# Kernel tuning notes

Measured on AMD Instinct MI355X. Metric: run time of the kernel, lower is better.

Reference implementation:

```python
import jax, jax.numpy as jnp
import numpy as np

IMG_W = 224
STRIDE = 16
NUM_HEADS = 12
# 196 grid centers, x-major order: [(x, y) for x in ... for y in ...]
_xs = np.arange(STRIDE // 2, IMG_W, STRIDE)
GRIDS = jnp.asarray(np.array([(x, y) for x in _xs for y in _xs], dtype=np.float32))  # [196, 2]


def setup_inputs() -> dict:
    key = jax.random.key(0)
    ks = jax.random.split(key, 8)
    B, N, C = 256, 198, 768
    s = 0.02
    return {
        "x": jax.random.normal(ks[0], (B, N, C), dtype=jnp.float32),
        "w_qkv": jax.random.normal(ks[1], (C, 3 * C), dtype=jnp.float32) * s,  # qkv_bias=False
        "w_proj": jax.random.normal(ks[2], (C, C), dtype=jnp.float32) * s,
        "b_proj": jax.random.normal(ks[3], (C,), dtype=jnp.float32) * s,
        "w_D": jax.random.normal(ks[4], (C, 3), dtype=jnp.float32) * s,
        "b_D": jax.random.normal(ks[5], (3,), dtype=jnp.float32) * s,
        "w_cen": jax.random.normal(ks[6], (C, 6), dtype=jnp.float32) * s,
        "b_cen": jax.random.normal(ks[7], (6,), dtype=jnp.float32) * s,
    }


def reference(x, w_qkv, w_proj, b_proj, w_D, b_D, w_cen, b_cen):
    B, N, C = x.shape
    H = NUM_HEADS
    dh = C // H
    scale = dh ** (-0.5)

    qkv = (x @ w_qkv).reshape(B, N, 3, H, dh).transpose(2, 0, 3, 1, 4)  # [3,B,H,N,dh]
    q, k, v = qkv[0], qkv[1], qkv[2]

    attn = jnp.einsum('bhnd,bhmd->bhnm', q, k) * scale
    attn = jax.nn.softmax(attn, axis=-1)  # [B,H,N,N]

    # CLS-token query, heads concatenated: q.permute(2,0,1,3).reshape(N,B,C)[0]
    q0 = q[:, :, 0, :].reshape(B, C)
    D = IMG_W * jax.nn.sigmoid(q0 @ w_D + b_D)                      # [B,3]
    cen = jax.nn.sigmoid((q0 @ w_cen + b_cen).reshape(B, 3, 2))     # [B,3,2]

    # mixture-of-gaussian blobs over 196 patch grid positions
    sigma = (D / 2.0)[..., None]                                    # [B,3,1]
    coord = cen * (IMG_W - 1)                                       # [B,3,2]
    dist = ((coord[:, :, None, :] - GRIDS[None, None]) ** 2).sum(-1)  # [B,3,196]
    mgb = jnp.exp(-dist / (2.0 * sigma ** 2)) / 2.0 / 3.14 / sigma ** 2
    mgb = mgb / mgb.sum(-1, keepdims=True)
    mgb = mgb.sum(axis=1) / 3.0                                     # [B,196]
    mgb = jnp.concatenate([jnp.ones((B, 2), mgb.dtype), mgb], axis=1)  # [B,N]

    # head-score reweighting of the CLS attention row
    hs = attn[:, :, 0, :].transpose(1, 0, 2)   # [H,B,N] == permute(1,2,0,3) squeezed
    hs = hs * mgb[None]                        # broadcast over heads
    hs = hs / hs.sum(-1, keepdims=True)
    # replicate torch masked_scatter flat-order semantics:
    # source flattened in (h,b,n) order is written into target positions in (b,h,n) order
    new_row = hs.reshape(-1).reshape(B, H, N)
    attn = attn.at[:, :, 0, :].set(new_row)

    out = jnp.einsum('bhnm,bhmd->bhnd', attn, v)      # [B,H,N,dh]
    out = out.transpose(0, 2, 1, 3).reshape(B, N, C)
    out = out @ w_proj + b_proj
    return cen, attn[:, :, 0, :], out
```

## Files before the change

kernel.cpp:

```cpp
#include <hip/hip_runtime.h>
#include <cstdint>
#include <cstddef>

typedef __attribute__((ext_vector_type(4))) float  f32x4;
typedef __attribute__((ext_vector_type(8))) __bf16 bf16x8;
typedef __attribute__((ext_vector_type(4))) __bf16 bf16x4;

#define MFMA16(A, B, C) __builtin_amdgcn_mfma_f32_16x16x32_bf16((A), (B), (C), 0, 0, 0)

#define GLOAD_LDS16(gp, lp)                                        \
    __builtin_amdgcn_global_load_lds(                              \
        (const __attribute__((address_space(1))) void*)(gp),       \
        (__attribute__((address_space(3))) void*)(lp), 16, 0, 0)

#define NB 256
#define NN 198
#define NC 768
#define NH 12

__global__ __launch_bounds__(256) void cast_to_bf16(const float* __restrict__ in,
                                                    __bf16* __restrict__ out, int n8) {
    int i = blockIdx.x * 256 + threadIdx.x;
    if (i < n8) {
        const float4 f0 = reinterpret_cast<const float4*>(in)[i * 2];
        const float4 f1 = reinterpret_cast<const float4*>(in)[i * 2 + 1];
        bf16x8 h;
        h[0] = (__bf16)f0.x; h[1] = (__bf16)f0.y; h[2] = (__bf16)f0.z; h[3] = (__bf16)f0.w;
        h[4] = (__bf16)f1.x; h[5] = (__bf16)f1.y; h[6] = (__bf16)f1.z; h[7] = (__bf16)f1.w;
        reinterpret_cast<bf16x8*>(out)[i] = h;
    }
}

__global__ __launch_bounds__(256) void transpose_to_bf16(
    const float* __restrict__ in, __bf16* __restrict__ out, int R, int Cc) {
    __shared__ __bf16 tile[32][33];
    const int ntc = Cc >> 5;
    const int tc = blockIdx.x % ntc, tr = blockIdx.x / ntc;
    const int c0 = tc * 32, r0 = tr * 32;
    const int lx = threadIdx.x & 31, ly = threadIdx.x >> 5;
#pragma unroll
    for (int j = 0; j < 4; ++j)
        tile[ly + j * 8][lx] = (__bf16)in[(size_t)(r0 + ly + j * 8) * Cc + c0 + lx];
    __syncthreads();
#pragma unroll
    for (int j = 0; j < 4; ++j)
        out[(size_t)(c0 + ly + j * 8) * R + r0 + lx] = tile[lx][ly + j * 8];
}

__global__ __launch_bounds__(512, 2) void gemm_qkv_v7(
    const __bf16* __restrict__ xb, const __bf16* __restrict__ wT,
    __bf16* __restrict__ qb, __bf16* __restrict__ kb, __bf16* __restrict__ vb,
    float* __restrict__ q0) {
    __shared__ __bf16 As[2][256 * 64];
    __shared__ __bf16 Bs[2][256 * 64];
    const int bid = blockIdx.x;
    const int xcd = bid & 7, lin = bid >> 3;
    const int wgid = (xcd < 6 ? xcd * 223 : 6 * 223 + (xcd - 6) * 222) + lin;
    const int brow = (wgid / 9) * 256;
    const int bcol = (wgid % 9) * 256;
    const int tid = threadIdx.x, lane = tid & 63, wid = tid >> 6;
    const int wr = wid >> 2, wc = wid & 3;
    const int lr = lane & 15, lg = lane >> 4;

    const int srow = tid >> 3;
    const int sslot = (tid & 7) ^ ((tid >> 3) & 7);
    const __bf16* aSrc = xb + (size_t)(brow + srow) * 768 + sslot * 8;
    const __bf16* bSrc = wT + (size_t)(bcol + srow) * 768 + sslot * 8;
    const int key = lr & 7;

    f32x4 acc[8][4] = {};

#define STAGE7(buf, kk0)                                                       \
    {                                                                          \
        __bf16* aD = &As[buf][wid * 512];                                      \
        __bf16* bD = &Bs[buf][wid * 512];                                      \
        _Pragma("unroll")                                                      \
        for (int j = 0; j < 4; ++j) {                                          \
            GLOAD_LDS16(aSrc + (size_t)j * 64 * 768 + (kk0), aD + j * 4096);   \
            GLOAD_LDS16(bSrc + (size_t)j * 64 * 768 + (kk0), bD + j * 4096);   \
        }                                                                      \
    }

#define LDA7(f0, f1, f2, f3, m0)                                               \
    f0 = *reinterpret_cast<const bf16x8*>(                                     \
        Ab + (wr * 128 + (m0) * 16 + lr) * 64 + ((lg ^ key) * 8));             \
    f1 = *reinterpret_cast<const bf16x8*>(                                     \
        Ab + (wr * 128 + (m0) * 16 + lr) * 64 + (((4 + lg) ^ key) * 8));       \
    f2 = *reinterpret_cast<const bf16x8*>(                                     \
        Ab + (wr * 128 + (m0) * 16 + 16 + lr) * 64 + ((lg ^ key) * 8));        \
    f3 = *reinterpret_cast<const bf16x8*>(                                     \
        Ab + (wr * 128 + (m0) * 16 + 16 + lr) * 64 + (((4 + lg) ^ key) * 8));

#define MFMA_PHASE7(f0, f1, f2, f3, m0)                                        \
    __builtin_amdgcn_s_setprio(1);                                             \
    _Pragma("unroll")                                                          \
    for (int nt = 0; nt < 4; ++nt) acc[(m0)][nt]     = MFMA16(f0, bfr[0][nt], acc[(m0)][nt]);     \
    _Pragma("unroll")                                                          \
    for (int nt = 0; nt < 4; ++nt) acc[(m0)][nt]     = MFMA16(f1, bfr[1][nt], acc[(m0)][nt]);     \
    _Pragma("unroll")                                                          \
    for (int nt = 0; nt < 4; ++nt) acc[(m0) + 1][nt] = MFMA16(f2, bfr[0][nt], acc[(m0) + 1][nt]); \
    _Pragma("unroll")                                                          \
    for (int nt = 0; nt < 4; ++nt) acc[(m0) + 1][nt] = MFMA16(f3, bfr[1][nt], acc[(m0) + 1][nt]); \
    __builtin_amdgcn_s_setprio(0);

    STAGE7(0, 0);
    STAGE7(1, 64);
    for (int tau = 0; tau < 12; ++tau) {
        const int b = tau & 1;
        if (tau == 11) asm volatile("s_waitcnt vmcnt(0)" ::: "memory");
        else           asm volatile("s_waitcnt vmcnt(8)" ::: "memory");
        __builtin_amdgcn_s_barrier();
        __builtin_amdgcn_sched_barrier(0);
        const __bf16* Ab = As[b];
        const __bf16* Bb = Bs[b];
        bf16x8 bfr[2][4];
#pragma unroll
        for (int kk = 0; kk < 2; ++kk)
#pragma unroll
            for (int nt = 0; nt < 4; ++nt)
                bfr[kk][nt] = *reinterpret_cast<const bf16x8*>(
                    Bb + (wc * 64 + nt * 16 + lr) * 64 + (((kk * 4 + lg) ^ key) * 8));
        bf16x8 a0, a1, a2, a3, b0, b1, b2, b3;
        LDA7(a0, a1, a2, a3, 0);
        LDA7(b0, b1, b2, b3, 2);
        asm volatile("s_waitcnt lgkmcnt(4)" ::: "memory");
        __builtin_amdgcn_sched_barrier(0);
        MFMA_PHASE7(a0, a1, a2, a3, 0);
        LDA7(a0, a1, a2, a3, 4);
        asm volatile("s_waitcnt lgkmcnt(4)" ::: "memory");
        __builtin_amdgcn_sched_barrier(0);
        MFMA_PHASE7(b0, b1, b2, b3, 2);
        LDA7(b0, b1, b2, b3, 6);
        asm volatile("s_waitcnt lgkmcnt(4)" ::: "memory");
        __builtin_amdgcn_sched_barrier(0);
        MFMA_PHASE7(a0, a1, a2, a3, 4);
        asm volatile("s_waitcnt lgkmcnt(0)" ::: "memory");
        __builtin_amdgcn_sched_barrier(0);
        __builtin_amdgcn_s_barrier();
        __builtin_amdgcn_sched_barrier(0);
        if (tau < 10) STAGE7(b, (tau + 2) * 64);
        MFMA_PHASE7(b0, b1, b2, b3, 6);
    }
#undef STAGE7

#pragma unroll
    for (int mt = 0; mt < 8; ++mt) {
        int grow0 = brow + wr * 128 + mt * 16 + lg * 4;
#pragma unroll
        for (int nt = 0; nt < 4; ++nt) {
            int gcol = bcol + wc * 64 + nt * 16 + lr;
            int sidx = gcol / 768;
            int rem  = gcol % 768;
            __bf16* dstbuf = (sidx == 0) ? qb : (sidx == 1) ? kb : vb;
            int hh = rem >> 6, dd = rem & 63;
#pragma unroll
            for (int r = 0; r < 4; ++r) {
                int grow = grow0 + r;
                int bb = grow / 198, nn2 = grow % 198;
                float val = acc[mt][nt][r];
                dstbuf[(((size_t)bb * 12 + hh) * 198 + nn2) * 64 + dd] = (__bf16)val;
                if (sidx == 0 && nn2 == 0) q0[bb * 768 + rem] = val;
            }
        }
    }
}

__global__ __launch_bounds__(256) void mgb_kernel(
    const float* __restrict__ q0, const float* __restrict__ wD,
    const float* __restrict__ bD, const float* __restrict__ wcen,
    const float* __restrict__ bcen, float* __restrict__ cen_out,
    float* __restrict__ mgb) {
    const int b = blockIdx.x, t = threadIdx.x;
    __shared__ float qs[768];
    __shared__ float red[256];
    __shared__ float vals[9];
    qs[t]       = q0[b * 768 + t];
    qs[t + 256] = q0[b * 768 + t + 256];
    qs[t + 512] = q0[b * 768 + t + 512];
    __syncthreads();
    for (int j = 0; j < 9; ++j) {
        float p;
        if (j < 3)
            p = qs[t] * wD[t * 3 + j] + qs[t + 256] * wD[(t + 256) * 3 + j] +
                qs[t + 512] * wD[(t + 512) * 3 + j];
        else {
            int c = j - 3;
            p = qs[t] * wcen[t * 6 + c] + qs[t + 256] * wcen[(t + 256) * 6 + c] +
                qs[t + 512] * wcen[(t + 512) * 6 + c];
        }
        red[t] = p;
        __syncthreads();
        for (int off = 128; off > 0; off >>= 1) {
            if (t < off) red[t] += red[t + off];
            __syncthreads();
        }
        if (t == 0) {
            float bias = (j < 3) ? bD[j] : bcen[j - 3];
            vals[j] = 1.f / (1.f + __expf(-(red[0] + bias)));
        }
        __syncthreads();
    }
    if (t < 6) cen_out[b * 6 + t] = vals[3 + t];

    float e3[3] = {0.f, 0.f, 0.f};
    if (t < 196) {
        float gx = 8.f + 16.f * (float)(t / 14);
        float gy = 8.f + 16.f * (float)(t % 14);
#pragma unroll
        for (int j = 0; j < 3; ++j) {
            float sig = 112.f * vals[j];
            float cx = vals[3 + 2 * j] * 223.f;
            float cy = vals[3 + 2 * j + 1] * 223.f;
            float dx = cx - gx, dy = cy - gy;
            e3[j] = __expf(-(dx * dx + dy * dy) / (2.f * sig * sig));
        }
    }
    float js[3];
    for (int j = 0; j < 3; ++j) {
        red[t] = e3[j];
        __syncthreads();
        for (int off = 128; off > 0; off >>= 1) {
            if (t < off) red[t] += red[t + off];
            __syncthreads();
        }
        js[j] = red[0];
        __syncthreads();
    }
    if (t < 196) {
        float m = (e3[0] / js[0] + e3[1] / js[1] + e3[2] / js[2]) * (1.f / 3.f);
        mgb[(size_t)b * 198 + 2 + t] = m;
    }
    if (t < 2) mgb[(size_t)b * 198 + t] = 1.f;
}

__global__ __launch_bounds__(256) void attn_kernel(
    const __bf16* __restrict__ qb, const __bf16* __restrict__ kb,
    const __bf16* __restrict__ vb, float* __restrict__ p0,
    __bf16* __restrict__ outp) {
    __shared__ __bf16 Vt[64][216];
    __shared__ __bf16 Plds[4][16][216];
    const int bh = blockIdx.x;
    const int b = bh / 12, h = bh % 12;
    const __bf16* Qp = qb + (size_t)bh * NN * 64;
    const __bf16* Kp = kb + (size_t)bh * NN * 64;
    const __bf16* Vp = vb + (size_t)bh * NN * 64;
    const int tid = threadIdx.x, lane = tid & 63, wid = tid >> 6;
    const int lr = lane & 15, lg = lane >> 4;

    for (int i = tid; i < 104 * 8; i += 256) {
        int key2 = (i >> 3) * 2, d0 = (i & 7) << 3;
        int kr0 = key2 < 198 ? key2 : 197;
        int kr1 = key2 + 1 < 198 ? key2 + 1 : 197;
        bf16x8 h0 = *reinterpret_cast<const bf16x8*>(Vp + kr0 * 64 + d0);
        bf16x8 h1 = *reinterpret_cast<const bf16x8*>(Vp + kr1 * 64 + d0);
#pragma unroll
        for (int j = 0; j < 8; ++j) {
            union { __bf16 hh[2]; unsigned u; } pk;
            pk.hh[0] = h0[j]; pk.hh[1] = h1[j];
            *reinterpret_cast<unsigned*>(&Vt[d0 + j][key2]) = pk.u;
        }
    }
    __syncthreads();

    for (int ch = wid; ch < 13; ch += 4) {
        int n0 = ch * 16;
        int qrow = n0 + lr; if (qrow > 197) qrow = 197;
        bf16x8 qf0 = *reinterpret_cast<const bf16x8*>(Qp + qrow * 64 + lg * 8);
        bf16x8 qf1 = *reinterpret_cast<const bf16x8*>(Qp + qrow * 64 + 32 + lg * 8);
        f32x4 sa[13];
#pragma unroll
        for (int t2 = 0; t2 < 13; ++t2) {
            int krow = t2 * 16 + lr; if (krow > 197) krow = 197;
            bf16x8 kf0 = *reinterpret_cast<const bf16x8*>(Kp + krow * 64 + lg * 8);
            bf16x8 kf1 = *reinterpret_cast<const bf16x8*>(Kp + krow * 64 + 32 + lg * 8);
            f32x4 a = (f32x4){0.f, 0.f, 0.f, 0.f};
            a = MFMA16(kf0, qf0, a);
            a = MFMA16(kf1, qf1, a);
            sa[t2] = a;
        }
        float rmax = -1e30f;
#pragma unroll
        for (int t2 = 0; t2 < 13; ++t2)
#pragma unroll
            for (int r = 0; r < 4; ++r) {
                int key = t2 * 16 + lg * 4 + r;
                float vv = (key < 198) ? sa[t2][r] * 0.125f : -1e30f;
                sa[t2][r] = vv;
                rmax = fmaxf(rmax, vv);
            }
        rmax = fmaxf(rmax, __shfl_xor(rmax, 16));
        rmax = fmaxf(rmax, __shfl_xor(rmax, 32));
        float rsum = 0.f;
#pragma unroll
        for (int t2 = 0; t2 < 13; ++t2)
#pragma unroll
            for (int r = 0; r < 4; ++r) {
                float e = __expf(sa[t2][r] - rmax);
                sa[t2][r] = e;
                rsum += e;
            }
        rsum += __shfl_xor(rsum, 16);
        rsum += __shfl_xor(rsum, 32);
        float inv = 1.f / rsum;

        if (ch == 0 && lr == 0) {
#pragma unroll
            for (int t2 = 0; t2 < 13; ++t2)
#pragma unroll
                for (int r = 0; r < 4; ++r) {
                    int key = t2 * 16 + lg * 4 + r;
                    if (key < 198) p0[(size_t)bh * 198 + key] = sa[t2][r] * inv;
                }
        }
#pragma unroll
        for (int t2 = 0; t2 < 13; ++t2) {
            bf16x4 pk;
#pragma unroll
            for (int r = 0; r < 4; ++r) pk[r] = (__bf16)(sa[t2][r] * inv);
            *reinterpret_cast<bf16x4*>(&Plds[wid][lr][t2 * 16 + lg * 4]) = pk;
        }
        asm volatile("s_waitcnt lgkmcnt(0)" ::: "memory");

        f32x4 o[4];
#pragma unroll
        for (int mt = 0; mt < 4; ++mt) o[mt] = (f32x4){0.f, 0.f, 0.f, 0.f};
#pragma unroll
        for (int ks = 0; ks < 7; ++ks) {
            int kbase = ks * 32 + lg * 8;
            bf16x8 pf;
            if (kbase < 208)
                pf = *reinterpret_cast<const bf16x8*>(&Plds[wid][lr][kbase]);
            else {
#pragma unroll
                for (int j = 0; j < 8; ++j) pf[j] = (__bf16)0.f;
            }
#pragma unroll
            for (int mt = 0; mt < 4; ++mt) {
                bf16x8 vf;
                if (kbase < 208)
                    vf = *reinterpret_cast<const bf16x8*>(&Vt[mt * 16 + lr][kbase]);
                else {
#pragma unroll
                    for (int j = 0; j < 8; ++j) vf[j] = (__bf16)0.f;
                }
                o[mt] = MFMA16(vf, pf, o[mt]);
            }
        }
        int qg = n0 + lr;
        if (qg < 198) {
            __bf16* dst = outp + ((size_t)b * 198 + qg) * 768 + h * 64;
#pragma unroll
            for (int mt = 0; mt < 4; ++mt) {
                bf16x4 pk;
#pragma unroll
                for (int r = 0; r < 4; ++r) pk[r] = (__bf16)o[mt][r];
                *reinterpret_cast<bf16x4*>(dst + mt * 16 + lg * 4) = pk;
            }
        }
    }
}

__global__ __launch_bounds__(64) void reweight_kernel(
    const float* __restrict__ p0, const float* __restrict__ mgb,
    const __bf16* __restrict__ vb, float* __restrict__ attn_out,
    __bf16* __restrict__ outp) {
    const int t = blockIdx.x;
    const int b = t / 12, h = t % 12;
    const int h2 = t >> 8, b2 = t & 255;
    const int lane = threadIdx.x;
    __shared__ float nr[198];
    const float* pr = p0 + (size_t)(b2 * 12 + h2) * 198;
    const float* mr = mgb + (size_t)b2 * 198;
    float w[4];
    float ssum = 0.f;
#pragma unroll
    for (int i = 0; i < 4; ++i) {
        int n = lane + 64 * i;
        float xv = (n < 198) ? pr[n] * mr[n] : 0.f;
        w[i] = xv;
        ssum += xv;
    }
#pragma unroll
    for (int m = 1; m < 64; m <<= 1) ssum += __shfl_xor(ssum, m);
    float inv = 1.f / ssum;
#pragma unroll
    for (int i = 0; i < 4; ++i) {
        int n = lane + 64 * i;
        if (n < 198) {
            float xv = w[i] * inv;
            nr[n] = xv;
            attn_out[(size_t)t * 198 + n] = xv;
        }
    }
    __syncthreads();
    const __bf16* vp = vb + (size_t)t * 198 * 64;
    float acc = 0.f;
    for (int n = 0; n < 198; ++n) acc += nr[n] * (float)vp[n * 64 + lane];
    outp[((size_t)b * 198) * 768 + h * 64 + lane] = (__bf16)acc;
}

__global__ __launch_bounds__(512, 2) void gemm_proj_v7(
    const __bf16* __restrict__ A, const __bf16* __restrict__ wT,
    const float* __restrict__ bias, float* __restrict__ out) {
    __shared__ __bf16 As[2][256 * 64];
    __shared__ __bf16 Bs[2][256 * 64];
    const int bid = blockIdx.x;
    const int xcd = bid & 7, lin = bid >> 3;
    const int wgid = (xcd < 2 ? xcd * 75 : 2 * 75 + (xcd - 2) * 74) + lin;
    const int brow = (wgid / 3) * 256;
    const int bcol = (wgid % 3) * 256;
    const int tid = threadIdx.x, lane = tid & 63, wid = tid >> 6;
    const int wr = wid >> 2, wc = wid & 3;
    const int lr = lane & 15, lg = lane >> 4;

    const int srow = tid >> 3;
    const int sslot = (tid & 7) ^ ((tid >> 3) & 7);
    const __bf16* aSrc = A  + (size_t)(brow + srow) * 768 + sslot * 8;
    const __bf16* bSrc = wT + (size_t)(bcol + srow) * 768 + sslot * 8;
    const int key = lr & 7;

    f32x4 acc[8][4] = {};

#define STAGE8(buf, kk0)                                                       \
    {                                                                          \
        __bf16* aD = &As[buf][wid * 512];                                      \
        __bf16* bD = &Bs[buf][wid * 512];                                      \
        _Pragma("unroll")                                                      \
        for (int j = 0; j < 4; ++j) {                                          \
            GLOAD_LDS16(aSrc + (size_t)j * 64 * 768 + (kk0), aD + j * 4096);   \
            GLOAD_LDS16(bSrc + (size_t)j * 64 * 768 + (kk0), bD + j * 4096);   \
        }                                                                      \
    }

    STAGE8(0, 0);
    STAGE8(1, 64);
    for (int tau = 0; tau < 12; ++tau) {
        const int b = tau & 1;
        if (tau == 11) asm volatile("s_waitcnt vmcnt(0)" ::: "memory");
        else           asm volatile("s_waitcnt vmcnt(8)" ::: "memory");
        __builtin_amdgcn_s_barrier();
        __builtin_amdgcn_sched_barrier(0);
        const __bf16* Ab = As[b];
        const __bf16* Bb = Bs[b];
        bf16x8 bfr[2][4];
#pragma unroll
        for (int kk = 0; kk < 2; ++kk)
#pragma unroll
            for (int nt = 0; nt < 4; ++nt)
                bfr[kk][nt] = *reinterpret_cast<const bf16x8*>(
                    Bb + (wc * 64 + nt * 16 + lr) * 64 + (((kk * 4 + lg) ^ key) * 8));
        bf16x8 a0, a1, a2, a3, b0, b1, b2, b3;
        LDA7(a0, a1, a2, a3, 0);
        LDA7(b0, b1, b2, b3, 2);
        asm volatile("s_waitcnt lgkmcnt(4)" ::: "memory");
        __builtin_amdgcn_sched_barrier(0);
        MFMA_PHASE7(a0, a1, a2, a3, 0);
        LDA7(a0, a1, a2, a3, 4);
        asm volatile("s_waitcnt lgkmcnt(4)" ::: "memory");
        __builtin_amdgcn_sched_barrier(0);
        MFMA_PHASE7(b0, b1, b2, b3, 2);
        LDA7(b0, b1, b2, b3, 6);
        asm volatile("s_waitcnt lgkmcnt(4)" ::: "memory");
        __builtin_amdgcn_sched_barrier(0);
        MFMA_PHASE7(a0, a1, a2, a3, 4);
        asm volatile("s_waitcnt lgkmcnt(0)" ::: "memory");
        __builtin_amdgcn_sched_barrier(0);
        __builtin_amdgcn_s_barrier();
        __builtin_amdgcn_sched_barrier(0);
        if (tau < 10) STAGE8(b, (tau + 2) * 64);
        MFMA_PHASE7(b0, b1, b2, b3, 6);
    }
#undef STAGE8

#pragma unroll
    for (int mt = 0; mt < 8; ++mt) {
#pragma unroll
        for (int nt = 0; nt < 4; ++nt) {
            int gcol = bcol + wc * 64 + nt * 16 + lr;
            float bv = bias[gcol];
#pragma unroll
            for (int r = 0; r < 4; ++r) {
                int grow = brow + wr * 128 + mt * 16 + lg * 4 + r;
                out[(size_t)grow * 768 + gcol] = acc[mt][nt][r] + bv;
            }
        }
    }
}

extern "C" void kernel_launch(void* const* d_in, const int* in_sizes, int n_in,
                              void* d_out, int out_size, void* d_ws, size_t ws_size,
                              hipStream_t stream) {
    const float* x      = (const float*)d_in[0];
    const float* w_qkv  = (const float*)d_in[1];
    const float* w_proj = (const float*)d_in[2];
    const float* b_proj = (const float*)d_in[3];
    const float* w_D    = (const float*)d_in[4];
    const float* b_D    = (const float*)d_in[5];
    const float* w_cen  = (const float*)d_in[6];
    const float* b_cen  = (const float*)d_in[7];

    float* out      = (float*)d_out;
    float* cen_out  = out;
    float* attn_out = out + 1536;
    float* proj_out = out + 1536 + 608256;

    char* ws = (char*)d_ws;
    size_t off = 0;
    auto carve = [&](size_t bytes) {
        void* p = ws + off;
        off += (bytes + 255) & ~(size_t)255;
        return p;
    };
    __bf16* wqkvT  = (__bf16*)carve((size_t)2304 * 768 * 2);
    __bf16* wprojT = (__bf16*)carve((size_t)768 * 768 * 2);
    __bf16* qb     = (__bf16*)carve((size_t)3072 * 198 * 64 * 2);
    __bf16* kb     = (__bf16*)carve((size_t)3072 * 198 * 64 * 2);
    __bf16* vb     = (__bf16*)carve((size_t)3072 * 198 * 64 * 2);
    __bf16* outp   = (__bf16*)carve((size_t)50688 * 768 * 2);
    float*  q0     = (float*)carve((size_t)256 * 768 * 4);
    float*  mgb    = (float*)carve((size_t)256 * 198 * 4);
    float*  p0     = (float*)carve((size_t)3072 * 198 * 4);

    __bf16* xb = outp;

    cast_to_bf16<<<(50688 * 768 / 8 + 255) / 256, 256, 0, stream>>>(x, xb, 50688 * 768 / 8);
    transpose_to_bf16<<<(2304 / 32) * (768 / 32), 256, 0, stream>>>(w_qkv, wqkvT, 768, 2304);
    transpose_to_bf16<<<(768 / 32) * (768 / 32), 256, 0, stream>>>(w_proj, wprojT, 768, 768);
    gemm_qkv_v7<<<1782, 512, 0, stream>>>(xb, wqkvT, qb, kb, vb, q0);
    mgb_kernel<<<256, 256, 0, stream>>>(q0, w_D, b_D, w_cen, b_cen, cen_out, mgb);
    attn_kernel<<<3072, 256, 0, stream>>>(qb, kb, vb, p0, outp);
    reweight_kernel<<<3072, 64, 0, stream>>>(p0, mgb, vb, attn_out, outp);
    gemm_proj_v7<<<594, 512, 0, stream>>>(outp, wprojT, b_proj, proj_out);
}
```

Before: 524.0 us.

## Pair query chunks for shared K fragments in attention; retile projection GEMM to 128x128

In the attention kernel each wave now computes QK^T for two query chunks at once, so every K fragment loaded from global memory feeds both chunks and K traffic is roughly halved. Softmax and PV move into a shared helper. Separately, the projection GEMM is rebuilt with 128x128 tiles, a K step of 32, 256 threads and 2376 blocks, plus s_setprio around the MFMAs. This trades per-block data reuse for more blocks and higher occupancy, while the attention change raises register pressure.

```diff
diff --git a/kernel.cpp b/kernel.cpp
--- a/kernel.cpp
+++ b/kernel.cpp
@@ -233,6 +233,91 @@
     if (t < 2) mgb[(size_t)b * 198 + t] = 1.f;
 }
 
+__device__ __forceinline__ void softmax_pv(
+    f32x4 (&sa)[13], int ch, int wid, int lr, int lg, int bh, int b, int h,
+    float* __restrict__ p0, __bf16* __restrict__ outp,
+    __bf16 (&Vt)[64][216], __bf16 (&Plds)[4][16][216]) {
+    float rmax = -1e30f;
+#pragma unroll
+    for (int t2 = 0; t2 < 13; ++t2)
+#pragma unroll
+        for (int r = 0; r < 4; ++r) {
+            int key = t2 * 16 + lg * 4 + r;
+            float vv = (key < 198) ? sa[t2][r] * 0.125f : -1e30f;
+            sa[t2][r] = vv;
+            rmax = fmaxf(rmax, vv);
+        }
+    rmax = fmaxf(rmax, __shfl_xor(rmax, 16));
+    rmax = fmaxf(rmax, __shfl_xor(rmax, 32));
+    float rsum = 0.f;
+#pragma unroll
+    for (int t2 = 0; t2 < 13; ++t2)
+#pragma unroll
+        for (int r = 0; r < 4; ++r) {
+            float e = __expf(sa[t2][r] - rmax);
+            sa[t2][r] = e;
+            rsum += e;
+        }
+    rsum += __shfl_xor(rsum, 16);
+    rsum += __shfl_xor(rsum, 32);
+    float inv = 1.f / rsum;
+
+    if (ch == 0 && lr == 0) {
+#pragma unroll
+        for (int t2 = 0; t2 < 13; ++t2)
+#pragma unroll
+            for (int r = 0; r < 4; ++r) {
+                int key = t2 * 16 + lg * 4 + r;
+                if (key < 198) p0[(size_t)bh * 198 + key] = sa[t2][r] * inv;
+            }
+    }
+#pragma unroll
+    for (int t2 = 0; t2 < 13; ++t2) {
+        bf16x4 pk;
+#pragma unroll
+        for (int r = 0; r < 4; ++r) pk[r] = (__bf16)(sa[t2][r] * inv);
+        *reinterpret_cast<bf16x4*>(&Plds[wid][lr][t2 * 16 + lg * 4]) = pk;
+    }
+    asm volatile("s_waitcnt lgkmcnt(0)" ::: "memory");
+
+    f32x4 o[4];
+#pragma unroll
+    for (int mt = 0; mt < 4; ++mt) o[mt] = (f32x4){0.f, 0.f, 0.f, 0.f};
+#pragma unroll
+    for (int ks = 0; ks < 7; ++ks) {
+        int kbase = ks * 32 + lg * 8;
+        bf16x8 pf;
+        if (kbase < 208)
+            pf = *reinterpret_cast<const bf16x8*>(&Plds[wid][lr][kbase]);
+        else {
+#pragma unroll
+            for (int j = 0; j < 8; ++j) pf[j] = (__bf16)0.f;
+        }
+#pragma unroll
+        for (int mt = 0; mt < 4; ++mt) {
+            bf16x8 vf;
+            if (kbase < 208)
+                vf = *reinterpret_cast<const bf16x8*>(&Vt[mt * 16 + lr][kbase]);
+            else {
+#pragma unroll
+                for (int j = 0; j < 8; ++j) vf[j] = (__bf16)0.f;
+            }
+            o[mt] = MFMA16(vf, pf, o[mt]);
+        }
+    }
+    int qg = ch * 16 + lr;
+    if (qg < 198) {
+        __bf16* dst = outp + ((size_t)b * 198 + qg) * 768 + h * 64;
+#pragma unroll
+        for (int mt = 0; mt < 4; ++mt) {
+            bf16x4 pk;
+#pragma unroll
+            for (int r = 0; r < 4; ++r) pk[r] = (__bf16)o[mt][r];
+            *reinterpret_cast<bf16x4*>(dst + mt * 16 + lg * 4) = pk;
+        }
+    }
+}
+
 __global__ __launch_bounds__(256) void attn_kernel(
     const __bf16* __restrict__ qb, const __bf16* __restrict__ kb,
     const __bf16* __restrict__ vb, float* __restrict__ p0,
@@ -262,101 +347,37 @@
     }
     __syncthreads();
 
-    for (int ch = wid; ch < 13; ch += 4) {
-        int n0 = ch * 16;
-        int qrow = n0 + lr; if (qrow > 197) qrow = 197;
-        bf16x8 qf0 = *reinterpret_cast<const bf16x8*>(Qp + qrow * 64 + lg * 8);
-        bf16x8 qf1 = *reinterpret_cast<const bf16x8*>(Qp + qrow * 64 + 32 + lg * 8);
-        f32x4 sa[13];
+#pragma unroll
+    for (int pp = 0; pp < 2; ++pp) {
+        const int c0 = wid + pp * 8;
+        const int c1 = c0 + 4;
+        const bool has1 = (c1 < 13);
+        int qrow0 = c0 * 16 + lr; if (qrow0 > 197) qrow0 = 197;
+        bf16x8 qf00 = *reinterpret_cast<const bf16x8*>(Qp + qrow0 * 64 + lg * 8);
+        bf16x8 qf01 = *reinterpret_cast<const bf16x8*>(Qp + qrow0 * 64 + 32 + lg * 8);
+        int qrow1 = has1 ? c1 * 16 + lr : 197; if (qrow1 > 197) qrow1 = 197;
+        bf16x8 qf10 = *reinterpret_cast<const bf16x8*>(Qp + qrow1 * 64 + lg * 8);
+        bf16x8 qf11 = *reinterpret_cast<const bf16x8*>(Qp + qrow1 * 64 + 32 + lg * 8);
+        f32x4 sa0[13], sa1[13];
 #pragma unroll
         for (int t2 = 0; t2 < 13; ++t2) {
             int krow = t2 * 16 + lr; if (krow > 197) krow = 197;
             bf16x8 kf0 = *reinterpret_cast<const bf16x8*>(Kp + krow * 64 + lg * 8);
             bf16x8 kf1 = *reinterpret_cast<const bf16x8*>(Kp + krow * 64 + 32 + lg * 8);
             f32x4 a = (f32x4){0.f, 0.f, 0.f, 0.f};
-            a = MFMA16(kf0, qf0, a);
-            a = MFMA16(kf1, qf1, a);
-            sa[t2] = a;
-        }
-        float rmax = -1e30f;
-#pragma unroll
-        for (int t2 = 0; t2 < 13; ++t2)
-#pragma unroll
-            for (int r = 0; r < 4; ++r) {
-                int key = t2 * 16 + lg * 4 + r;
-                float vv = (key < 198) ? sa[t2][r] * 0.125f : -1e30f;
-                sa[t2][r] = vv;
-                rmax = fmaxf(rmax, vv);
+            a = MFMA16(kf0, qf00, a);
+            a = MFMA16(kf1, qf01, a);
+            sa0[t2] = a;
+            if (has1) {
+                f32x4 c = (f32x4){0.f, 0.f, 0.f, 0.f};
+                c = MFMA16(kf0, qf10, c);
+                c = MFMA16(kf1, qf11, c);
+                sa1[t2] = c;
             }
-        rmax = fmaxf(rmax, __shfl_xor(rmax, 16));
-        rmax = fmaxf(rmax, __shfl_xor(rmax, 32));
-        float rsum = 0.f;
-#pragma unroll
-        for (int t2 = 0; t2 < 13; ++t2)
-#pragma unroll
-            for (int r = 0; r < 4; ++r) {
-                float e = __expf(sa[t2][r] - rmax);
-                sa[t2][r] = e;
-                rsum += e;
-            }
-        rsum += __shfl_xor(rsum, 16);
-        rsum += __shfl_xor(rsum, 32);
-        float inv = 1.f / rsum;
-
-        if (ch == 0 && lr == 0) {
-#pragma unroll
-            for (int t2 = 0; t2 < 13; ++t2)
-#pragma unroll
-                for (int r = 0; r < 4; ++r) {
-                    int key = t2 * 16 + lg * 4 + r;
-                    if (key < 198) p0[(size_t)bh * 198 + key] = sa[t2][r] * inv;
-                }
-        }
-#pragma unroll
-        for (int t2 = 0; t2 < 13; ++t2) {
-            bf16x4 pk;
-#pragma unroll
-            for (int r = 0; r < 4; ++r) pk[r] = (__bf16)(sa[t2][r] * inv);
-            *reinterpret_cast<bf16x4*>(&Plds[wid][lr][t2 * 16 + lg * 4]) = pk;
-        }
-        asm volatile("s_waitcnt lgkmcnt(0)" ::: "memory");
-
-        f32x4 o[4];
-#pragma unroll
-        for (int mt = 0; mt < 4; ++mt) o[mt] = (f32x4){0.f, 0.f, 0.f, 0.f};
-#pragma unroll
-        for (int ks = 0; ks < 7; ++ks) {
-            int kbase = ks * 32 + lg * 8;
-            bf16x8 pf;
-            if (kbase < 208)
-                pf = *reinterpret_cast<const bf16x8*>(&Plds[wid][lr][kbase]);
-            else {
-#pragma unroll
-                for (int j = 0; j < 8; ++j) pf[j] = (__bf16)0.f;
-            }
-#pragma unroll
-            for (int mt = 0; mt < 4; ++mt) {
-                bf16x8 vf;
-                if (kbase < 208)
-                    vf = *reinterpret_cast<const bf16x8*>(&Vt[mt * 16 + lr][kbase]);
-                else {
-#pragma unroll
-                    for (int j = 0; j < 8; ++j) vf[j] = (__bf16)0.f;
-                }
-                o[mt] = MFMA16(vf, pf, o[mt]);
-            }
-        }
-        int qg = n0 + lr;
-        if (qg < 198) {
-            __bf16* dst = outp + ((size_t)b * 198 + qg) * 768 + h * 64;
-#pragma unroll
-            for (int mt = 0; mt < 4; ++mt) {
-                bf16x4 pk;
-#pragma unroll
-                for (int r = 0; r < 4; ++r) pk[r] = (__bf16)o[mt][r];
-                *reinterpret_cast<bf16x4*>(dst + mt * 16 + lg * 4) = pk;
-            }
-        }
+        }
+        softmax_pv(sa0, c0, wid, lr, lg, bh, b, h, p0, outp, Vt, Plds);
+        if (has1)
+            softmax_pv(sa1, c1, wid, lr, lg, bh, b, h, p0, outp, Vt, Plds);
     }
 }
 
@@ -399,88 +420,84 @@
     outp[((size_t)b * 198) * 768 + h * 64 + lane] = (__bf16)acc;
 }
 
-__global__ __launch_bounds__(512, 2) void gemm_proj_v7(
+__global__ __launch_bounds__(256, 3) void gemm_proj_v8(
     const __bf16* __restrict__ A, const __bf16* __restrict__ wT,
     const float* __restrict__ bias, float* __restrict__ out) {
-    __shared__ __bf16 As[2][256 * 64];
-    __shared__ __bf16 Bs[2][256 * 64];
+    __shared__ __bf16 As[2][128 * 32];
+    __shared__ __bf16 Bs[2][128 * 32];
     const int bid = blockIdx.x;
-    const int xcd = bid & 7, lin = bid >> 3;
-    const int wgid = (xcd < 2 ? xcd * 75 : 2 * 75 + (xcd - 2) * 74) + lin;
-    const int brow = (wgid / 3) * 256;
-    const int bcol = (wgid % 3) * 256;
+    const int wg  = (bid & 7) * 297 + (bid >> 3);
+    const int brow = (wg / 6) * 128;
+    const int bcol = (wg % 6) * 128;
     const int tid = threadIdx.x, lane = tid & 63, wid = tid >> 6;
-    const int wr = wid >> 2, wc = wid & 3;
+    const int wm = wid >> 1, wn = wid & 1;
     const int lr = lane & 15, lg = lane >> 4;
 
-    const int srow = tid >> 3;
-    const int sslot = (tid & 7) ^ ((tid >> 3) & 7);
+    const int srow = tid >> 2;
+    const int sslot = (tid & 3) ^ ((tid >> 3) & 3);
     const __bf16* aSrc = A  + (size_t)(brow + srow) * 768 + sslot * 8;
     const __bf16* bSrc = wT + (size_t)(bcol + srow) * 768 + sslot * 8;
-    const int key = lr & 7;
-
-    f32x4 acc[8][4] = {};
-
-#define STAGE8(buf, kk0)                                                       \
-    {                                                                          \
-        __bf16* aD = &As[buf][wid * 512];                                      \
-        __bf16* bD = &Bs[buf][wid * 512];                                      \
-        _Pragma("unroll")                                                      \
-        for (int j = 0; j < 4; ++j) {                                          \
-            GLOAD_LDS16(aSrc + (size_t)j * 64 * 768 + (kk0), aD + j * 4096);   \
-            GLOAD_LDS16(bSrc + (size_t)j * 64 * 768 + (kk0), bD + j * 4096);   \
-        }                                                                      \
-    }
-
-    STAGE8(0, 0);
-    STAGE8(1, 64);
-    for (int tau = 0; tau < 12; ++tau) {
-        const int b = tau & 1;
-        if (tau == 11) asm volatile("s_waitcnt vmcnt(0)" ::: "memory");
-        else           asm volatile("s_waitcnt vmcnt(8)" ::: "memory");
+    const int rkey = (lr >> 1) & 3;
+
+    f32x4 acc[4][4] = {};
+
+#define STAGE_P6(buf, kk0)                                                    \
+    {                                                                         \
+        __bf16* aD = &As[buf][wid * 512];                                     \
+        __bf16* bD = &Bs[buf][wid * 512];                                     \
+        GLOAD_LDS16(aSrc + (kk0), aD);                                        \
+        GLOAD_LDS16(bSrc + (kk0), bD);                                        \
+        GLOAD_LDS16(aSrc + (size_t)64 * 768 + (kk0), aD + 2048);              \
+        GLOAD_LDS16(bSrc + (size_t)64 * 768 + (kk0), bD + 2048);              \
+    }
+
+#define COMPUTE_P6(buf)                                                       \
+    {                                                                         \
+        const __bf16* Ab = As[buf];                                           \
+        const __bf16* Bb = Bs[buf];                                           \
+        bf16x8 af[4], bfv[4];                                                 \
+        _Pragma("unroll")                                                     \
+        for (int nt = 0; nt < 4; ++nt)                                        \
+            bfv[nt] = *reinterpret_cast<const bf16x8*>(                       \
+                Bb + (wn * 64 + nt * 16 + lr) * 32 + ((lg ^ rkey) * 8));      \
+        _Pragma("unroll")                                                     \
+        for (int mt = 0; mt < 4; ++mt)                                        \
+            af[mt] = *reinterpret_cast<const bf16x8*>(                        \
+                Ab + (wm * 64 + mt * 16 + lr) * 32 + ((lg ^ rkey) * 8));      \
+        __builtin_amdgcn_s_setprio(1);                                        \
+        _Pragma("unroll")                                                     \
+        for (int mt = 0; mt < 4; ++mt)                                        \
+            _Pragma("unroll")                                                 \
+            for (int nt = 0; nt < 4; ++nt)                                    \
+                acc[mt][nt] = MFMA16(af[mt], bfv[nt], acc[mt][nt]);           \
+        __builtin_amdgcn_s_setprio(0);                                        \
+    }
+
+    STAGE_P6(0, 0);
+    STAGE_P6(1, 32);
+    for (int tau = 0; tau < 24; ++tau) {
+        if (tau == 23) asm volatile("s_waitcnt vmcnt(0)" ::: "memory");
+        else           asm volatile("s_waitcnt vmcnt(4)" ::: "memory");
         __builtin_amdgcn_s_barrier();
         __builtin_amdgcn_sched_barrier(0);
-        const __bf16* Ab = As[b];
-        const __bf16* Bb = Bs[b];
-        bf16x8 bfr[2][4];
-#pragma unroll
-        for (int kk = 0; kk < 2; ++kk)
-#pragma unroll
-            for (int nt = 0; nt < 4; ++nt)
-                bfr[kk][nt] = *reinterpret_cast<const bf16x8*>(
-                    Bb + (wc * 64 + nt * 16 + lr) * 64 + (((kk * 4 + lg) ^ key) * 8));
-        bf16x8 a0, a1, a2, a3, b0, b1, b2, b3;
-        LDA7(a0, a1, a2, a3, 0);
-        LDA7(b0, b1, b2, b3, 2);
-        asm volatile("s_waitcnt lgkmcnt(4)" ::: "memory");
-        __builtin_amdgcn_sched_barrier(0);
-        MFMA_PHASE7(a0, a1, a2, a3, 0);
-        LDA7(a0, a1, a2, a3, 4);
-        asm volatile("s_waitcnt lgkmcnt(4)" ::: "memory");
-        __builtin_amdgcn_sched_barrier(0);
-        MFMA_PHASE7(b0, b1, b2, b3, 2);
-        LDA7(b0, b1, b2, b3, 6);
-        asm volatile("s_waitcnt lgkmcnt(4)" ::: "memory");
-        __builtin_amdgcn_sched_barrier(0);
-        MFMA_PHASE7(a0, a1, a2, a3, 4);
-        asm volatile("s_waitcnt lgkmcnt(0)" ::: "memory");
+        COMPUTE_P6(tau & 1);
         __builtin_amdgcn_sched_barrier(0);
         __builtin_amdgcn_s_barrier();
         __builtin_amdgcn_sched_barrier(0);
-        if (tau < 10) STAGE8(b, (tau + 2) * 64);
-        MFMA_PHASE7(b0, b1, b2, b3, 6);
-    }
-#undef STAGE8
-
-#pragma unroll
-    for (int mt = 0; mt < 8; ++mt) {
+        if (tau < 22) STAGE_P6(tau & 1, (tau + 2) * 32);
+    }
+#undef STAGE_P6
+#undef COMPUTE_P6
+
+#pragma unroll
+    for (int mt = 0; mt < 4; ++mt) {
 #pragma unroll
         for (int nt = 0; nt < 4; ++nt) {
-            int gcol = bcol + wc * 64 + nt * 16 + lr;
+            int gcol = bcol + wn * 64 + nt * 16 + lr;
             float bv = bias[gcol];
 #pragma unroll
             for (int r = 0; r < 4; ++r) {
-                int grow = brow + wr * 128 + mt * 16 + lg * 4 + r;
+                int grow = brow + wm * 64 + mt * 16 + lg * 4 + r;
                 out[(size_t)grow * 768 + gcol] = acc[mt][nt][r] + bv;
             }
         }
@@ -530,5 +547,5 @@
     mgb_kernel<<<256, 256, 0, stream>>>(q0, w_D, b_D, w_cen, b_cen, cen_out, mgb);
     attn_kernel<<<3072, 256, 0, stream>>>(qb, kb, vb, p0, outp);
     reweight_kernel<<<3072, 64, 0, stream>>>(p0, mgb, vb, attn_out, outp);
-    gemm_proj_v7<<<594, 512, 0, stream>>>(outp, wprojT, b_proj, proj_out);
-}
+    gemm_proj_v8<<<2376, 256, 0, stream>>>(outp, wprojT, b_proj, proj_out);
+}
```

New measurement: 640.9 us. 22.3% more time.
